# Kernel tuning notes

Measured on AMD Instinct MI355X. Metric: run time of the kernel, lower is better.

The kernel has to match this reference:

```python
import jax, jax.numpy as jnp
import numpy as np

KEY_DIM = 512
VALUE_DIM = 128
CAPACITY = 500000
N_RETRIEVE = 32
LN_EPS = 1e-5       # torch nn.LayerNorm default
NORM_EPS = 1e-12    # torch F.normalize default


def setup_inputs() -> dict:
    key = jax.random.key(0)
    ks = jax.random.split(key, 5)
    w_scale = 0.02
    return {
        "query": jax.random.normal(ks[0], (1, KEY_DIM), dtype=jnp.float32),
        "W1": jax.random.normal(ks[1], (KEY_DIM, KEY_DIM), dtype=jnp.float32) * w_scale,
        "b1": jnp.zeros((KEY_DIM,), dtype=jnp.float32),
        "W2": jax.random.normal(ks[2], (KEY_DIM, KEY_DIM), dtype=jnp.float32) * w_scale,
        "b2": jnp.zeros((KEY_DIM,), dtype=jnp.float32),
        "ln_g": jnp.ones((KEY_DIM,), dtype=jnp.float32),
        "ln_b": jnp.zeros((KEY_DIM,), dtype=jnp.float32),
        "keys": jax.random.normal(ks[3], (CAPACITY, KEY_DIM), dtype=jnp.float32),
        "values": jax.random.normal(ks[4], (CAPACITY, VALUE_DIM), dtype=jnp.float32),
    }


def _l2_normalize(x, axis=-1):
    # matches torch F.normalize: x / max(||x||, eps)
    n = jnp.linalg.norm(x, axis=axis, keepdims=True)
    return x / jnp.maximum(n, NORM_EPS)


def _layer_norm(x, g, b):
    mu = jnp.mean(x, axis=-1, keepdims=True)
    var = jnp.mean(jnp.square(x - mu), axis=-1, keepdims=True)
    return (x - mu) * jax.lax.rsqrt(var + LN_EPS) * g + b


def reference(query, W1, b1, W2, b2, ln_g, ln_b, keys, values):
    # EpisodicMemory.read_aggregated with a full memory bank (n == capacity).
    q_in = jax.lax.stop_gradient(query)                 # query.detach()
    h = jax.nn.silu(q_in @ W1.T + b1) @ W2.T + b2       # key_proj MLP, [1, K]
    h = _layer_norm(h, ln_g, ln_b)                      # key_norm
    q = _l2_normalize(h)[0]                             # [K]
    kn = _l2_normalize(keys)                            # [C, K]
    sim = kn @ q                                        # cosine sims, [C]
    top_sim, top_idx = jax.lax.top_k(sim, N_RETRIEVE)   # [k], [k]
    vals = values[top_idx]                              # gather, [k, V]
    attn = jax.nn.softmax(top_sim, axis=0)              # [k]
    return jnp.sum(vals * attn[:, None], axis=0)        # [V]
```

## Files before the change

kernel.cpp:

```cpp
#include <hip/hip_runtime.h>
#include <hip/hip_bf16.h>
#include <math.h>

#define KEY_DIM   512
#define VALUE_DIM 128
#define CAPACITY  500000
#define NRET      32
#define LN_EPS    1e-5f
#define NORM_EPS  1e-12f
#define NEG_INF   (-3.402823466e38f)

#define SCAN_BLOCKS 1024
#define CHUNK       489


__device__ inline float blockSum512(float v, float* red) {
  #pragma unroll
  for (int off = 32; off; off >>= 1) v += __shfl_xor(v, off);
  int wid = threadIdx.x >> 6, lane = threadIdx.x & 63;
  if (lane == 0) red[wid] = v;
  __syncthreads();
  float s = red[0] + red[1] + red[2] + red[3] + red[4] + red[5] + red[6] + red[7];
  __syncthreads();
  return s;
}

__device__ inline void waveArgMax3(float& v, int& gi, int& code) {
  #pragma unroll
  for (int off = 32; off; off >>= 1) {
    float ov = __shfl_xor(v, off);
    int   og = __shfl_xor(gi, off);
    int   oc = __shfl_xor(code, off);
    if (ov > v || (ov == v && og < gi)) { v = ov; gi = og; code = oc; }
  }
}


__global__ __launch_bounds__(256) void matvec1_kernel(
    const float* __restrict__ query, const float* __restrict__ W1,
    const float* __restrict__ b1, float* __restrict__ h)
{
  int tid = threadIdx.x, wid = tid >> 6, lane = tid & 63;
  int row = (blockIdx.x << 2) + wid;
  const float4* q4 = (const float4*)query;
  const float4* wrow = (const float4*)(W1 + (size_t)row * KEY_DIM);
  float4 a0 = wrow[lane],      q0 = q4[lane];
  float4 a1 = wrow[lane + 64], q1 = q4[lane + 64];
  float acc = a0.x*q0.x + a0.y*q0.y + a0.z*q0.z + a0.w*q0.w
            + a1.x*q1.x + a1.y*q1.y + a1.z*q1.z + a1.w*q1.w;
  #pragma unroll
  for (int off = 32; off; off >>= 1) acc += __shfl_xor(acc, off);
  if (lane == 0) {
    float x = acc + b1[row];
    h[row] = x / (1.f + expf(-x));
  }
}

__global__ __launch_bounds__(256) void matvec2_kernel(
    const float* __restrict__ h, const float* __restrict__ W2,
    const float* __restrict__ b2, float* __restrict__ g)
{
  int tid = threadIdx.x, wid = tid >> 6, lane = tid & 63;
  int row = (blockIdx.x << 2) + wid;
  const float4* h4 = (const float4*)h;
  const float4* wrow = (const float4*)(W2 + (size_t)row * KEY_DIM);
  float4 a0 = wrow[lane],      q0 = h4[lane];
  float4 a1 = wrow[lane + 64], q1 = h4[lane + 64];
  float acc = a0.x*q0.x + a0.y*q0.y + a0.z*q0.z + a0.w*q0.w
            + a1.x*q1.x + a1.y*q1.y + a1.z*q1.z + a1.w*q1.w;
  #pragma unroll
  for (int off = 32; off; off >>= 1) acc += __shfl_xor(acc, off);
  if (lane == 0) g[row] = acc + b2[row];
}

__global__ __launch_bounds__(512) void norm_kernel(
    const float* __restrict__ g, const float* __restrict__ ln_g,
    const float* __restrict__ ln_b, float* __restrict__ qn)
{
  __shared__ float red[8];
  int tid = threadIdx.x;
  float x  = g[tid];
  float mu = blockSum512(x, red) * (1.f / 512.f);
  float d  = x - mu;
  float var = blockSum512(d * d, red) * (1.f / 512.f);
  float y  = d * (1.f / sqrtf(var + LN_EPS)) * ln_g[tid] + ln_b[tid];
  float nsq = blockSum512(y * y, red);
  float n  = fmaxf(sqrtf(nsq), NORM_EPS);
  qn[tid] = y / n;
}


__global__ __launch_bounds__(256) void scan_topk(
    const float* __restrict__ keys, const float* __restrict__ qn,
    float* __restrict__ cand_val, int* __restrict__ cand_idx, int C)
{
  int tid = threadIdx.x, wid = tid >> 6, lane = tid & 63;
  int s0  = blockIdx.x * CHUNK;
  int cnt = min(CHUNK, C - s0);
  int nrow = (cnt > wid) ? ((cnt - wid + 3) >> 2) : 0;

  const float4* q4 = (const float4*)qn;
  float4 q0 = q4[lane];
  float4 q1 = q4[lane + 64];
  const float4* keys4 = (const float4*)keys;

  float v0 = NEG_INF, v1 = NEG_INF;

  #pragma unroll 2
  for (int j = 0; j < nrow; ++j) {
    size_t rb = (size_t)(s0 + wid + (j << 2)) * 128;
    float4 a = keys4[rb + lane];
    float4 c = keys4[rb + 64 + lane];
    float dot = a.x*q0.x + a.y*q0.y + a.z*q0.z + a.w*q0.w
              + c.x*q1.x + c.y*q1.y + c.z*q1.z + c.w*q1.w;
    float ss  = a.x*a.x + a.y*a.y + a.z*a.z + a.w*a.w
              + c.x*c.x + c.y*c.y + c.z*c.z + c.w*c.w;
    #pragma unroll
    for (int off = 32; off; off >>= 1) {
      dot += __shfl_xor(dot, off);
      ss  += __shfl_xor(ss, off);
    }
    float sim = dot / fmaxf(sqrtf(ss), NORM_EPS);
    bool mine = (lane == (j & 63));
    if (j < 64) { if (mine) v0 = sim; }
    else        { if (mine) v1 = sim; }
  }

  int gbase = s0 + wid;
  int out0 = ((blockIdx.x << 2) + wid) * NRET;
  for (int it = 0; it < NRET; ++it) {
    bool pick1 = (v1 > v0);
    float v = pick1 ? v1 : v0;
    int slot = pick1 ? 1 : 0;
    int gi = gbase + ((lane + (slot << 6)) << 2);
    int code = (lane << 1) | slot;
    waveArgMax3(v, gi, code);
    if (lane == (code >> 1)) {
      if (code & 1) v1 = NEG_INF; else v0 = NEG_INF;
    }
    if (lane == 0) {
      cand_val[out0 + it] = v;
      cand_idx[out0 + it] = v > NEG_INF ? gi : 0x7ffffff0;
    }
  }
}


__global__ __launch_bounds__(256) void merge_topk(
    const float* __restrict__ in_val, const int* __restrict__ in_idx,
    float* __restrict__ out_val, int* __restrict__ out_idx)
{
  __shared__ float cv[1024];
  __shared__ int   ci[1024];
  __shared__ float redv[4];
  __shared__ int   redg[4];
  __shared__ int   redp[4];
  int tid = threadIdx.x, wid = tid >> 6, lane = tid & 63;
  int base = blockIdx.x << 10;
  for (int t = tid; t < 1024; t += 256) { cv[t] = in_val[base + t]; ci[t] = in_idx[base + t]; }
  __syncthreads();

  for (int it = 0; it < NRET; ++it) {
    float bv = NEG_INF; int bg = 0x7fffffff; int bp = -1;
    #pragma unroll
    for (int k = 0; k < 4; ++k) {
      int p = tid + (k << 8);
      float vv = cv[p]; int gg = ci[p];
      if (vv > bv || (vv == bv && gg < bg)) { bv = vv; bg = gg; bp = p; }
    }
    waveArgMax3(bv, bg, bp);
    if (lane == 0) { redv[wid] = bv; redg[wid] = bg; redp[wid] = bp; }
    __syncthreads();
    if (tid == 0) {
      float v = redv[0]; int g = redg[0]; int p = redp[0];
      #pragma unroll
      for (int i = 1; i < 4; ++i)
        if (redv[i] > v || (redv[i] == v && redg[i] < g)) { v = redv[i]; g = redg[i]; p = redp[i]; }
      out_val[(blockIdx.x << 5) + it] = v;
      out_idx[(blockIdx.x << 5) + it] = g;
      if (p >= 0) cv[p] = NEG_INF;
    }
    __syncthreads();
  }
}


__global__ __launch_bounds__(256) void final_kernel(
    const float* __restrict__ c3v, const int* __restrict__ c3i,
    const float* __restrict__ values, float* __restrict__ out)
{
  __shared__ float cv[128];
  __shared__ int   ci[128];
  __shared__ float selv[NRET];
  __shared__ int   seli[NRET];
  __shared__ float attn[NRET];
  int tid = threadIdx.x, wid = tid >> 6, lane = tid & 63;
  if (tid < 128) { cv[tid] = c3v[tid]; ci[tid] = c3i[tid]; }
  __syncthreads();

  if (wid == 0) {
    float v0 = cv[lane], v1 = cv[lane + 64];
    int   g0 = ci[lane], g1 = ci[lane + 64];
    for (int it = 0; it < NRET; ++it) {
      bool pick1 = (v1 > v0) || (v1 == v0 && g1 < g0);
      float v = pick1 ? v1 : v0;
      int  gi = pick1 ? g1 : g0;
      int code = (lane << 1) | (pick1 ? 1 : 0);
      waveArgMax3(v, gi, code);
      if (lane == (code >> 1)) {
        if (code & 1) v1 = NEG_INF; else v0 = NEG_INF;
      }
      if (lane == 0) { selv[it] = v; seli[it] = gi; }
    }
  }
  __syncthreads();

  if (wid == 0) {
    int idx = lane & 31;
    float e = expf(selv[idx] - selv[0]);
    float s = e;
    #pragma unroll
    for (int off = 16; off; off >>= 1) s += __shfl_xor(s, off);
    if (lane < 32) attn[lane] = e / s;
  }
  __syncthreads();

  if (tid < VALUE_DIM) {
    float acc = 0.f;
    #pragma unroll
    for (int k = 0; k < NRET; ++k)
      acc += attn[k] * values[(size_t)seli[k] * VALUE_DIM + tid];
    out[tid] = acc;
  }
}


extern "C" void kernel_launch(void* const* d_in, const int* in_sizes, int n_in,
                              void* d_out, int out_size, void* d_ws, size_t ws_size,
                              hipStream_t stream) {
  const float* query  = (const float*)d_in[0];
  const float* W1     = (const float*)d_in[1];
  const float* b1     = (const float*)d_in[2];
  const float* W2     = (const float*)d_in[3];
  const float* b2     = (const float*)d_in[4];
  const float* ln_g   = (const float*)d_in[5];
  const float* ln_b   = (const float*)d_in[6];
  const float* keys   = (const float*)d_in[7];
  const float* values = (const float*)d_in[8];
  float* out = (float*)d_out;

  float* wsf = (float*)d_ws;
  float* h        = wsf;
  float* g        = wsf + 512;
  float* qn       = wsf + 1024;
  float* cand_val = wsf + 2048;
  int*   cand_idx = (int*)(wsf + 2048 + 131072);
  float* c2v      = wsf + 2048 + 262144;
  int*   c2i      = (int*)(wsf + 2048 + 262144 + 4096);
  float* c3v      = wsf + 2048 + 262144 + 8192;
  int*   c3i      = (int*)(wsf + 2048 + 262144 + 8192 + 128);

  hipLaunchKernelGGL(matvec1_kernel, dim3(128), dim3(256), 0, stream, query, W1, b1, h);
  hipLaunchKernelGGL(matvec2_kernel, dim3(128), dim3(256), 0, stream, h, W2, b2, g);
  hipLaunchKernelGGL(norm_kernel,    dim3(1),   dim3(512), 0, stream, g, ln_g, ln_b, qn);
  hipLaunchKernelGGL(scan_topk,      dim3(SCAN_BLOCKS), dim3(256), 0, stream,
                     keys, qn, cand_val, cand_idx, CAPACITY);
  hipLaunchKernelGGL(merge_topk,     dim3(128), dim3(256), 0, stream,
                     cand_val, cand_idx, c2v, c2i);
  hipLaunchKernelGGL(merge_topk,     dim3(4),   dim3(256), 0, stream,
                     c2v, c2i, c3v, c3i);
  hipLaunchKernelGGL(final_kernel,   dim3(1),   dim3(256), 0, stream,
                     c3v, c3i, values, out);
}
```

Before: 309.0 us.

## Replace serial per-wave top-k extraction with bitonic sort and finer scan blocks

```diff
diff --git a/kernel.cpp b/kernel.cpp
--- a/kernel.cpp
+++ b/kernel.cpp
@@ -1,5 +1,4 @@
 #include <hip/hip_runtime.h>
-#include <hip/hip_bf16.h>
 #include <math.h>
 
 #define KEY_DIM   512
@@ -9,21 +8,39 @@
 #define LN_EPS    1e-5f
 #define NORM_EPS  1e-12f
 #define NEG_INF   (-3.402823466e38f)
-
-#define SCAN_BLOCKS 1024
-#define CHUNK       489
-
-
-__device__ inline float blockSum512(float v, float* red) {
-  #pragma unroll
-  for (int off = 32; off; off >>= 1) v += __shfl_xor(v, off);
-  int wid = threadIdx.x >> 6, lane = threadIdx.x & 63;
-  if (lane == 0) red[wid] = v;
-  __syncthreads();
-  float s = red[0] + red[1] + red[2] + red[3] + red[4] + red[5] + red[6] + red[7];
-  __syncthreads();
-  return s;
-}
+#define IDX_INF   0x7fffffff
+
+#define SCAN_BLOCKS 2048
+#define CHUNK       245
+#define JMAX        62
+
+
+template<int CTRL>
+__device__ inline float dppMovF(float x) {
+  return __int_as_float(__builtin_amdgcn_update_dpp(0, __float_as_int(x), CTRL, 0xF, 0xF, true));
+}
+
+__device__ inline float waveSumF(float x) {
+  x += dppMovF<0xB1>(x);
+  x += dppMovF<0x4E>(x);
+  x += dppMovF<0x124>(x);
+  x += dppMovF<0x128>(x);
+  x += __int_as_float(__builtin_amdgcn_ds_swizzle(__float_as_int(x), 0x401F));
+  x += __shfl_xor(x, 32);
+  return x;
+}
+
+template<int D>
+__device__ inline int fetchI(int x) {
+  if constexpr (D == 1)       return __builtin_amdgcn_update_dpp(0, x, 0xB1, 0xF, 0xF, true);
+  else if constexpr (D == 2)  return __builtin_amdgcn_update_dpp(0, x, 0x4E, 0xF, 0xF, true);
+  else if constexpr (D == 4)  return __builtin_amdgcn_ds_swizzle(x, 0x101F);
+  else if constexpr (D == 8)  return __builtin_amdgcn_ds_swizzle(x, 0x201F);
+  else if constexpr (D == 16) return __builtin_amdgcn_ds_swizzle(x, 0x401F);
+  else                        return __shfl_xor(x, 32);
+}
+template<int D>
+__device__ inline float fetchF(float x) { return __int_as_float(fetchI<D>(__float_as_int(x))); }
 
 __device__ inline void waveArgMax3(float& v, int& gi, int& code) {
   #pragma unroll
@@ -33,6 +50,17 @@
     int   oc = __shfl_xor(code, off);
     if (ov > v || (ov == v && og < gi)) { v = ov; gi = og; code = oc; }
   }
+}
+
+__device__ inline float blockSum512(float v, float* red) {
+  #pragma unroll
+  for (int off = 32; off; off >>= 1) v += __shfl_xor(v, off);
+  int wid = threadIdx.x >> 6, lane = threadIdx.x & 63;
+  if (lane == 0) red[wid] = v;
+  __syncthreads();
+  float s = red[0] + red[1] + red[2] + red[3] + red[4] + red[5] + red[6] + red[7];
+  __syncthreads();
+  return s;
 }
 
 
@@ -96,52 +124,55 @@
 {
   int tid = threadIdx.x, wid = tid >> 6, lane = tid & 63;
   int s0  = blockIdx.x * CHUNK;
-  int cnt = min(CHUNK, C - s0);
-  int nrow = (cnt > wid) ? ((cnt - wid + 3) >> 2) : 0;
 
   const float4* q4 = (const float4*)qn;
   float4 q0 = q4[lane];
   float4 q1 = q4[lane + 64];
   const float4* keys4 = (const float4*)keys;
 
-  float v0 = NEG_INF, v1 = NEG_INF;
+  float v  = NEG_INF;
+  int   gi = IDX_INF;
 
   #pragma unroll 2
-  for (int j = 0; j < nrow; ++j) {
-    size_t rb = (size_t)(s0 + wid + (j << 2)) * 128;
-    float4 a = keys4[rb + lane];
-    float4 c = keys4[rb + 64 + lane];
+  for (int j = 0; j < JMAX; ++j) {
+    int row   = s0 + wid + (j << 2);
+    bool valid = row < C;
+    int rc    = valid ? row : (C - 1);
+    const float4* kr = keys4 + (size_t)rc * 128;
+    float4 a = kr[lane];
+    float4 c = kr[lane + 64];
     float dot = a.x*q0.x + a.y*q0.y + a.z*q0.z + a.w*q0.w
               + c.x*q1.x + c.y*q1.y + c.z*q1.z + c.w*q1.w;
     float ss  = a.x*a.x + a.y*a.y + a.z*a.z + a.w*a.w
               + c.x*c.x + c.y*c.y + c.z*c.z + c.w*c.w;
-    #pragma unroll
-    for (int off = 32; off; off >>= 1) {
-      dot += __shfl_xor(dot, off);
-      ss  += __shfl_xor(ss, off);
+    dot = waveSumF(dot);
+    ss  = waveSumF(ss);
+    float sim = dot / fmaxf(sqrtf(ss), NORM_EPS);
+    if (lane == j) {
+      v  = valid ? sim : NEG_INF;
+      gi = valid ? row : IDX_INF;
     }
-    float sim = dot / fmaxf(sqrtf(ss), NORM_EPS);
-    bool mine = (lane == (j & 63));
-    if (j < 64) { if (mine) v0 = sim; }
-    else        { if (mine) v1 = sim; }
-  }
-
-  int gbase = s0 + wid;
-  int out0 = ((blockIdx.x << 2) + wid) * NRET;
-  for (int it = 0; it < NRET; ++it) {
-    bool pick1 = (v1 > v0);
-    float v = pick1 ? v1 : v0;
-    int slot = pick1 ? 1 : 0;
-    int gi = gbase + ((lane + (slot << 6)) << 2);
-    int code = (lane << 1) | slot;
-    waveArgMax3(v, gi, code);
-    if (lane == (code >> 1)) {
-      if (code & 1) v1 = NEG_INF; else v0 = NEG_INF;
-    }
-    if (lane == 0) {
-      cand_val[out0 + it] = v;
-      cand_idx[out0 + it] = v > NEG_INF ? gi : 0x7ffffff0;
-    }
+  }
+
+  #define BSTAGE(D, K) { \
+    float ov = fetchF<D>(v); int og = fetchI<D>(gi); \
+    bool keepL = ((lane & (D)) == 0) == ((lane & (K)) == 0); \
+    bool ogt = (ov > v) || (ov == v && og < gi); \
+    bool take = keepL ? ogt : !ogt; \
+    if (take) { v = ov; gi = og; } }
+
+  BSTAGE(1,2)
+  BSTAGE(2,4)  BSTAGE(1,4)
+  BSTAGE(4,8)  BSTAGE(2,8)  BSTAGE(1,8)
+  BSTAGE(8,16) BSTAGE(4,16) BSTAGE(2,16) BSTAGE(1,16)
+  BSTAGE(16,32) BSTAGE(8,32) BSTAGE(4,32) BSTAGE(2,32) BSTAGE(1,32)
+  BSTAGE(32,64) BSTAGE(16,64) BSTAGE(8,64) BSTAGE(4,64) BSTAGE(2,64) BSTAGE(1,64)
+  #undef BSTAGE
+
+  if (lane < NRET) {
+    int w = (blockIdx.x << 2) + wid;
+    cand_val[w * NRET + lane] = v;
+    cand_idx[w * NRET + lane] = gi;
   }
 }
 
@@ -161,7 +192,7 @@
   __syncthreads();
 
   for (int it = 0; it < NRET; ++it) {
-    float bv = NEG_INF; int bg = 0x7fffffff; int bp = -1;
+    float bv = NEG_INF; int bg = IDX_INF; int bp = -1;
     #pragma unroll
     for (int k = 0; k < 4; ++k) {
       int p = tid + (k << 8);
@@ -172,13 +203,13 @@
     if (lane == 0) { redv[wid] = bv; redg[wid] = bg; redp[wid] = bp; }
     __syncthreads();
     if (tid == 0) {
-      float v = redv[0]; int g = redg[0]; int p = redp[0];
+      float vv = redv[0]; int gg = redg[0]; int pp = redp[0];
       #pragma unroll
       for (int i = 1; i < 4; ++i)
-        if (redv[i] > v || (redv[i] == v && redg[i] < g)) { v = redv[i]; g = redg[i]; p = redp[i]; }
-      out_val[(blockIdx.x << 5) + it] = v;
-      out_idx[(blockIdx.x << 5) + it] = g;
-      if (p >= 0) cv[p] = NEG_INF;
+        if (redv[i] > vv || (redv[i] == vv && redg[i] < gg)) { vv = redv[i]; gg = redg[i]; pp = redp[i]; }
+      out_val[(blockIdx.x << 5) + it] = vv;
+      out_idx[(blockIdx.x << 5) + it] = gg;
+      if (pp >= 0) cv[pp] = NEG_INF;
     }
     __syncthreads();
   }
@@ -189,39 +220,37 @@
     const float* __restrict__ c3v, const int* __restrict__ c3i,
     const float* __restrict__ values, float* __restrict__ out)
 {
-  __shared__ float cv[128];
-  __shared__ int   ci[128];
   __shared__ float selv[NRET];
   __shared__ int   seli[NRET];
   __shared__ float attn[NRET];
   int tid = threadIdx.x, wid = tid >> 6, lane = tid & 63;
-  if (tid < 128) { cv[tid] = c3v[tid]; ci[tid] = c3i[tid]; }
-  __syncthreads();
 
   if (wid == 0) {
-    float v0 = cv[lane], v1 = cv[lane + 64];
-    int   g0 = ci[lane], g1 = ci[lane + 64];
+    float v0 = c3v[lane], v1 = c3v[lane + 64], v2 = c3v[lane + 128], v3 = c3v[lane + 192];
+    int   g0 = c3i[lane], g1 = c3i[lane + 64], g2 = c3i[lane + 128], g3 = c3i[lane + 192];
     for (int it = 0; it < NRET; ++it) {
-      bool pick1 = (v1 > v0) || (v1 == v0 && g1 < g0);
-      float v = pick1 ? v1 : v0;
-      int  gi = pick1 ? g1 : g0;
-      int code = (lane << 1) | (pick1 ? 1 : 0);
-      waveArgMax3(v, gi, code);
-      if (lane == (code >> 1)) {
-        if (code & 1) v1 = NEG_INF; else v0 = NEG_INF;
+      float bv = v0; int bg = g0; int bc = 0;
+      if (v1 > bv || (v1 == bv && g1 < bg)) { bv = v1; bg = g1; bc = 1; }
+      if (v2 > bv || (v2 == bv && g2 < bg)) { bv = v2; bg = g2; bc = 2; }
+      if (v3 > bv || (v3 == bv && g3 < bg)) { bv = v3; bg = g3; bc = 3; }
+      int code = (lane << 2) | bc;
+      waveArgMax3(bv, bg, code);
+      if (lane == (code >> 2)) {
+        int s = code & 3;
+        if (s == 0) v0 = NEG_INF; else if (s == 1) v1 = NEG_INF;
+        else if (s == 2) v2 = NEG_INF; else v3 = NEG_INF;
       }
-      if (lane == 0) { selv[it] = v; seli[it] = gi; }
+      if (lane == 0) { selv[it] = bv; seli[it] = bg; }
     }
   }
   __syncthreads();
 
-  if (wid == 0) {
-    int idx = lane & 31;
-    float e = expf(selv[idx] - selv[0]);
+  if (tid < NRET) {
+    float e = expf(selv[tid] - selv[0]);
     float s = e;
     #pragma unroll
     for (int off = 16; off; off >>= 1) s += __shfl_xor(s, off);
-    if (lane < 32) attn[lane] = e / s;
+    attn[tid] = e / s;
   }
   __syncthreads();
 
@@ -250,24 +279,24 @@
   float* out = (float*)d_out;
 
   float* wsf = (float*)d_ws;
-  float* h        = wsf;
-  float* g        = wsf + 512;
-  float* qn       = wsf + 1024;
+  float* qn       = wsf;
+  float* h        = wsf + 512;
+  float* g        = wsf + 1024;
   float* cand_val = wsf + 2048;
-  int*   cand_idx = (int*)(wsf + 2048 + 131072);
-  float* c2v      = wsf + 2048 + 262144;
-  int*   c2i      = (int*)(wsf + 2048 + 262144 + 4096);
-  float* c3v      = wsf + 2048 + 262144 + 8192;
-  int*   c3i      = (int*)(wsf + 2048 + 262144 + 8192 + 128);
+  int*   cand_idx = (int*)(wsf + 2048 + 262144);
+  float* c2v      = wsf + 2048 + 524288;
+  int*   c2i      = (int*)(wsf + 2048 + 524288 + 8192);
+  float* c3v      = wsf + 2048 + 524288 + 16384;
+  int*   c3i      = (int*)(wsf + 2048 + 524288 + 16384 + 256);
 
   hipLaunchKernelGGL(matvec1_kernel, dim3(128), dim3(256), 0, stream, query, W1, b1, h);
   hipLaunchKernelGGL(matvec2_kernel, dim3(128), dim3(256), 0, stream, h, W2, b2, g);
   hipLaunchKernelGGL(norm_kernel,    dim3(1),   dim3(512), 0, stream, g, ln_g, ln_b, qn);
   hipLaunchKernelGGL(scan_topk,      dim3(SCAN_BLOCKS), dim3(256), 0, stream,
                      keys, qn, cand_val, cand_idx, CAPACITY);
-  hipLaunchKernelGGL(merge_topk,     dim3(128), dim3(256), 0, stream,
+  hipLaunchKernelGGL(merge_topk,     dim3(256), dim3(256), 0, stream,
                      cand_val, cand_idx, c2v, c2i);
-  hipLaunchKernelGGL(merge_topk,     dim3(4),   dim3(256), 0, stream,
+  hipLaunchKernelGGL(merge_topk,     dim3(8),   dim3(256), 0, stream,
                      c2v, c2i, c3v, c3i);
   hipLaunchKernelGGL(final_kernel,   dim3(1),   dim3(256), 0, stream,
                      c3v, c3i, values, out);
```

Result: faster. 299.3 us (-3.1%).
